# Performance work log

Measured on AMD Instinct MI355X. Metric: run time of the kernel, lower is better.

The kernel has to match this reference:

```python
import jax, jax.numpy as jnp
import numpy as np

N = 10000      # nodes
E = 320000     # edges
F_IN = 33      # input node features
H = 32         # hidden
G = 64         # graphs in batch


def setup_inputs() -> dict:
    key = jax.random.key(0)
    ks = jax.random.split(key, 24)
    s = 0.1  # small init scale for numerical sanity
    inp = {
        "x": jax.random.normal(ks[0], (N, F_IN), jnp.float32),
        "edge_index": jax.random.randint(ks[1], (2, E), 0, N, jnp.int32),
        "edge_attr": jax.random.uniform(ks[2], (E, 1), jnp.float32),
        "batch": jnp.sort(jax.random.randint(ks[3], (N,), 0, G, jnp.int32)),
        # conv1: edge-MLP Linear(1 -> F_IN*H), root weight [F_IN,H], bias [H]
        "nn_w1": jax.random.normal(ks[4], (1, F_IN * H), jnp.float32) * s,
        "nn_b1": jax.random.normal(ks[5], (F_IN * H,), jnp.float32) * s,
        "root1": jax.random.normal(ks[6], (F_IN, H), jnp.float32) * s,
        "bias1": jnp.zeros((H,), jnp.float32),
        # conv2: edge-MLP Linear(1 -> H*H)
        "nn_w2": jax.random.normal(ks[7], (1, H * H), jnp.float32) * s,
        "nn_b2": jax.random.normal(ks[8], (H * H,), jnp.float32) * s,
        "root2": jax.random.normal(ks[9], (H, H), jnp.float32) * s,
        "bias2": jnp.zeros((H,), jnp.float32),
        # conv3
        "nn_w3": jax.random.normal(ks[10], (1, H * H), jnp.float32) * s,
        "nn_b3": jax.random.normal(ks[11], (H * H,), jnp.float32) * s,
        "root3": jax.random.normal(ks[12], (H, H), jnp.float32) * s,
        "bias3": jnp.zeros((H,), jnp.float32),
        # readout MLP: Linear(3H -> H), Linear(H -> 2)
        "lin1_w": jax.random.normal(ks[13], (3 * H, H), jnp.float32) * s,
        "lin1_b": jnp.zeros((H,), jnp.float32),
        "lin2_w": jax.random.normal(ks[14], (H, 2), jnp.float32) * s,
        "lin2_b": jnp.zeros((2,), jnp.float32),
    }
    return inp


def _nnconv(x, src, dst, edge_attr, nn_w, nn_b, root, bias):
    """PyG NNConv (aggr='add'): out_i = x_i @ root + bias + sum_{e: dst(e)=i} x_{src(e)} @ Theta(e_attr)."""
    in_dim, out_dim = root.shape
    # per-edge weight matrix from edge MLP: [E, in, out]
    W = (edge_attr @ nn_w + nn_b).reshape(-1, in_dim, out_dim)
    msg = jnp.einsum('ei,eio->eo', x[src], W)          # gather + per-edge small matmul
    agg = jax.ops.segment_sum(msg, dst, num_segments=N)  # scatter-add into targets
    return agg + x @ root + bias


def reference(x, edge_index, edge_attr, batch,
              nn_w1, nn_b1, root1, bias1,
              nn_w2, nn_b2, root2, bias2,
              nn_w3, nn_b3, root3, bias3,
              lin1_w, lin1_b, lin2_w, lin2_b):
    src, dst = edge_index[0], edge_index[1]
    h = jax.nn.relu(_nnconv(x, src, dst, edge_attr, nn_w1, nn_b1, root1, bias1))
    h = jax.nn.relu(_nnconv(h, src, dst, edge_attr, nn_w2, nn_b2, root2, bias2))
    h = jax.nn.relu(_nnconv(h, src, dst, edge_attr, nn_w3, nn_b3, root3, bias3))
    # global add / mean / max pooling over graphs
    add_p = jax.ops.segment_sum(h, batch, num_segments=G)
    cnt = jax.ops.segment_sum(jnp.ones((N, 1), h.dtype), batch, num_segments=G)
    mean_p = add_p / jnp.maximum(cnt, 1.0)
    max_p = jax.ops.segment_max(h, batch, num_segments=G)
    max_p = jnp.where(jnp.isfinite(max_p), max_p, 0.0)  # guard empty segments
    g = jnp.concatenate([add_p, mean_p, max_p], axis=1)  # [G, 3H]
    g = jax.nn.relu(g @ lin1_w + lin1_b)
    # dropout p=0.5 is identity in eval mode
    logits = g @ lin2_w + lin2_b
    return jax.nn.log_softmax(logits, axis=-1)
```

## Files before the change

kernel.cpp:

```cpp
#include <hip/hip_runtime.h>

constexpr int N_  = 10000;
constexpr int E_  = 320000;
constexpr int F1  = 33;
constexpr int H   = 32;
constexpr int G   = 64;
constexpr int CAP = 96;

constexpr int GRID = 1250;
constexpr int BT   = 256;

__device__ __forceinline__ unsigned bf16r(float x) {
    unsigned u = __float_as_uint(x);
    return (u + 0x7FFFu + ((u >> 16) & 1u)) >> 16;
}

struct Prm {
    const float* x; const int* ei; const float* ea; const int* batch;
    const float* A1; const float* B1; const float* R1; const float* z1;
    const float* A2; const float* B2; const float* R2; const float* z2;
    const float* A3; const float* B3; const float* R3; const float* z3;
    const float* l1w; const float* l1b; const float* l2w; const float* l2b;
    int* counts; int* startsP; unsigned* meta;
    unsigned* UVa; float* Ra; unsigned* UVb; float* Rb;
    float* psum; unsigned* pmax;
    float* out;
};

__global__ __launch_bounds__(BT, 5) void k_build(Prm p) {
    const int tid = threadIdx.x, bid = blockIdx.x;
    {
        int e = bid * BT + tid;
        int s = p.ei[e];
        int d = p.ei[E_ + e];
        float av = p.ea[e];
        int pos = atomicAdd(&p.counts[d], 1);
        p.meta[(size_t)d * CAP + pos] = (unsigned)s | (bf16r(av) << 16);
    }
    const int grp = tid >> 5, f = tid & 31;
    const int node = bid * 8 + grp;
    if (f == 0) {
        int b = p.batch[node];
        int bp = (node == 0) ? -1 : p.batch[node - 1];
        if (b != bp) p.startsP[b] = node + 1;
    }
    float u = 0.f, v = 0.f, r = p.z1[f];
    const float* xr = p.x + (size_t)node * F1;
    #pragma unroll
    for (int k = 0; k < F1; ++k) {
        float xv = xr[k];
        u = fmaf(xv, p.A1[k * H + f], u);
        v = fmaf(xv, p.B1[k * H + f], v);
        r = fmaf(xv, p.R1[k * H + f], r);
    }
    p.UVa[(node << 5) | f] = bf16r(u) | (bf16r(v) << 16);
    p.Ra [(node << 5) | f] = r;
}

template<int LAYER>
__global__ __launch_bounds__(BT, 5) void k_agg(Prm p) {
    __shared__ float wL[3][H * H];
    __shared__ float sh[8][H];
    const int tid = threadIdx.x;

    const unsigned* UVin; const float* Rin; unsigned* UVout; float* Rout;
    if (LAYER == 1)      { UVin = p.UVa; Rin = p.Ra; UVout = p.UVb; Rout = p.Rb; }
    else if (LAYER == 2) { UVin = p.UVb; Rin = p.Rb; UVout = p.UVa; Rout = p.Ra; }
    else                 { UVin = p.UVa; Rin = p.Ra; UVout = nullptr; Rout = nullptr; }

    if (LAYER == 1) {
        for (int i = tid; i < H * H; i += BT) {
            wL[0][i] = p.A2[i]; wL[1][i] = p.B2[i]; wL[2][i] = p.R2[i];
        }
        __syncthreads();
    } else if (LAYER == 2) {
        for (int i = tid; i < H * H; i += BT) {
            wL[0][i] = p.A3[i]; wL[1][i] = p.B3[i]; wL[2][i] = p.R3[i];
        }
        __syncthreads();
    }

    const int lane = tid & 63, wav = tid >> 6;
    const int l2 = lane & 31;
    const int rg = l2 >> 3;
    const int fq = l2 & 7;
    const int n = blockIdx.x * 8 + wav * 2 + (lane >> 5);
    const int dg = p.counts[n];
    const unsigned* mrow = p.meta + (size_t)n * CAP;
    unsigned m0 = mrow[l2];
    float r = Rin[(n << 5) | l2];

    float a0 = 0.f, a1 = 0.f, a2 = 0.f, a3 = 0.f;
    uint4 wq[8]; unsigned mq[8];

    auto issue = [&](unsigned mreg, int t, int sl) {
        int j = 4 * t + rg;
        unsigned mv = __shfl(mreg, (lane & 32) | (j & 31), 64);
        mq[sl] = mv;
        unsigned src = min(mv & 0xFFFFu, (unsigned)(N_ - 1));
        wq[sl] = *reinterpret_cast<const uint4*>(UVin + ((size_t)src << 5) + 4 * fq);
    };
    auto use = [&](int t, int sl) {
        unsigned mv = mq[sl]; uint4 w = wq[sl];
        float a = __uint_as_float(mv & 0xFFFF0000u);
        bool live = (4 * t + rg) < dg;
        float t0 = fmaf(a, __uint_as_float(w.x << 16), __uint_as_float(w.x & 0xFFFF0000u));
        float t1 = fmaf(a, __uint_as_float(w.y << 16), __uint_as_float(w.y & 0xFFFF0000u));
        float t2 = fmaf(a, __uint_as_float(w.z << 16), __uint_as_float(w.z & 0xFFFF0000u));
        float t3 = fmaf(a, __uint_as_float(w.w << 16), __uint_as_float(w.w & 0xFFFF0000u));
        if (live) { a0 += t0; a1 += t1; a2 += t2; a3 += t3; }
    };

    #pragma unroll
    for (int t = 0; t < 8; ++t) issue(m0, t, t);
    const bool need1 = __any(dg > 32);
    unsigned m1 = 0;
    if (need1) m1 = mrow[32 + l2];
    #pragma unroll
    for (int t = 0; t < 8; ++t) use(t, t);
    if (need1) {
        #pragma unroll
        for (int t = 8; t < 12; ++t) issue(m1, t, t - 8);
        #pragma unroll
        for (int t = 8; t < 12; ++t) use(t, t - 8);
        if (__any(dg > 48)) {
            #pragma unroll
            for (int t = 12; t < 16; ++t) issue(m1, t, t - 12);
            #pragma unroll
            for (int t = 12; t < 16; ++t) use(t, t - 12);
            if (__any(dg > 64)) {
                unsigned m2 = mrow[64 + l2];
                #pragma unroll
                for (int t = 16; t < 24; ++t) issue(m2, t, t - 16);
                #pragma unroll
                for (int t = 16; t < 24; ++t) use(t, t - 16);
            }
        }
    }

    a0 += __shfl_xor(a0, 8);  a0 += __shfl_xor(a0, 16);
    a1 += __shfl_xor(a1, 8);  a1 += __shfl_xor(a1, 16);
    a2 += __shfl_xor(a2, 8);  a2 += __shfl_xor(a2, 16);
    a3 += __shfl_xor(a3, 8);  a3 += __shfl_xor(a3, 16);

    int rsrc = (lane & 32) | (l2 >> 2);
    float s0 = __shfl(a0, rsrc, 64), s1 = __shfl(a1, rsrc, 64);
    float s2 = __shfl(a2, rsrc, 64), s3 = __shfl(a3, rsrc, 64);
    int c = l2 & 3;
    float accf = (c == 0) ? s0 : (c == 1) ? s1 : (c == 2) ? s2 : s3;

    float h = fmaxf(r + accf, 0.f);

    if (LAYER == 3) {
        sh[wav * 2 + (lane >> 5)][l2] = h;
        __syncthreads();
        if (tid < 32) {
            const int f = tid;
            const int n0 = blockIdx.x * 8;
            float s = 0.f, mx = 0.f;
            int cg = p.batch[n0];
            #pragma unroll
            for (int i = 0; i < 8; ++i) {
                int bg = p.batch[n0 + i];
                if (bg != cg) {
                    atomicAdd(&p.psum[cg * H + f], s);
                    atomicMax(&p.pmax[cg * H + f], __float_as_uint(mx));
                    s = 0.f; mx = 0.f; cg = bg;
                }
                float hv = sh[i][f];
                s += hv; mx = fmaxf(mx, hv);
            }
            atomicAdd(&p.psum[cg * H + f], s);
            atomicMax(&p.pmax[cg * H + f], __float_as_uint(mx));
        }
    } else {
        const float zf = (LAYER == 1) ? p.z2[l2] : p.z3[l2];
        float u = 0.f, v = 0.f, rn = zf;
        #pragma unroll
        for (int k = 0; k < H; ++k) {
            float hk = __shfl(h, k, 32);
            u  = fmaf(hk, wL[0][k * H + l2], u);
            v  = fmaf(hk, wL[1][k * H + l2], v);
            rn = fmaf(hk, wL[2][k * H + l2], rn);
        }
        UVout[(n << 5) | l2] = bf16r(u) | (bf16r(v) << 16);
        Rout [(n << 5) | l2] = rn;
    }
}

__global__ __launch_bounds__(64, 8) void k_read(Prm p) {
    __shared__ int   sst[G];
    __shared__ float gpl[3 * H];
    const int tid = threadIdx.x;
    const int g = blockIdx.x;
    sst[tid] = p.startsP[tid];
    __syncthreads();
    int sp = sst[g];
    int s0 = 0, e0 = 0;
    if (sp != 0) {
        s0 = sp - 1;
        e0 = N_;
        for (int j = g + 1; j < G; ++j)
            if (sst[j]) { e0 = sst[j] - 1; break; }
    }
    if (tid < 32) {
        float sum = p.psum[g * H + tid];
        float mx  = __uint_as_float(p.pmax[g * H + tid]);
        float c = fmaxf((float)(e0 - s0), 1.0f);
        gpl[tid] = sum;
        gpl[H + tid] = sum / c;
        gpl[2 * H + tid] = mx;
    }
    __syncthreads();
    if (tid < 32) {
        float hacc = p.l1b[tid];
        #pragma unroll
        for (int k = 0; k < H; ++k) {
            hacc = fmaf(gpl[k],         p.l1w[k * H + tid], hacc);
            hacc = fmaf(gpl[H + k],     p.l1w[(H + k) * H + tid], hacc);
            hacc = fmaf(gpl[2 * H + k], p.l1w[(2 * H + k) * H + tid], hacc);
        }
        float hid = fmaxf(hacc, 0.f);
        float p0 = hid * p.l2w[tid * 2 + 0];
        float p1 = hid * p.l2w[tid * 2 + 1];
        #pragma unroll
        for (int o = 16; o; o >>= 1) {
            p0 += __shfl_xor(p0, o, 32);
            p1 += __shfl_xor(p1, o, 32);
        }
        if (tid == 0) {
            float l0 = p0 + p.l2b[0], l1 = p1 + p.l2b[1];
            float m = fmaxf(l0, l1);
            float lse = m + logf(expf(l0 - m) + expf(l1 - m));
            p.out[g * 2 + 0] = l0 - lse;
            p.out[g * 2 + 1] = l1 - lse;
        }
    }
}


extern "C" void kernel_launch(void* const* d_in, const int* in_sizes, int n_in,
                              void* d_out, int out_size, void* d_ws, size_t ws_size,
                              hipStream_t stream) {
    const float* x      = (const float*)d_in[0];
    const int*   ei     = (const int*)  d_in[1];
    const float* ea     = (const float*)d_in[2];
    const int*   batch  = (const int*)  d_in[3];
    const float* nn_w1  = (const float*)d_in[4];
    const float* nn_b1  = (const float*)d_in[5];
    const float* root1  = (const float*)d_in[6];
    const float* bias1  = (const float*)d_in[7];
    const float* nn_w2  = (const float*)d_in[8];
    const float* nn_b2  = (const float*)d_in[9];
    const float* root2  = (const float*)d_in[10];
    const float* bias2  = (const float*)d_in[11];
    const float* nn_w3  = (const float*)d_in[12];
    const float* nn_b3  = (const float*)d_in[13];
    const float* root3  = (const float*)d_in[14];
    const float* bias3  = (const float*)d_in[15];
    const float* lin1_w = (const float*)d_in[16];
    const float* lin1_b = (const float*)d_in[17];
    const float* lin2_w = (const float*)d_in[18];
    const float* lin2_b = (const float*)d_in[19];
    float* out = (float*)d_out;

    char* ws = (char*)d_ws;
    size_t off = 0;
    auto alloc = [&](size_t bytes) -> void* {
        void* p = ws + off;
        off += (bytes + 255) & ~(size_t)255;
        return p;
    };
    const size_t zbytes = N_ * sizeof(int) + G * sizeof(int)
                        + G * H * sizeof(float) + G * H * sizeof(unsigned);
    char* zchunk = (char*)alloc(zbytes);
    int*      counts  = (int*)zchunk;
    int*      startsP = (int*)(zchunk + N_ * sizeof(int));
    float*    psum    = (float*)(zchunk + N_ * sizeof(int) + G * sizeof(int));
    unsigned* pmax    = (unsigned*)(zchunk + N_ * sizeof(int) + G * sizeof(int)
                                    + G * H * sizeof(float));
    unsigned* meta = (unsigned*)alloc((size_t)N_ * CAP * sizeof(unsigned));
    unsigned* UVa = (unsigned*)alloc((size_t)N_ * H * sizeof(unsigned));
    float*    Ra  = (float*)   alloc((size_t)N_ * H * sizeof(float));
    unsigned* UVb = (unsigned*)alloc((size_t)N_ * H * sizeof(unsigned));
    float*    Rb  = (float*)   alloc((size_t)N_ * H * sizeof(float));

    Prm prm{ x, ei, ea, batch,
             nn_w1, nn_b1, root1, bias1,
             nn_w2, nn_b2, root2, bias2,
             nn_w3, nn_b3, root3, bias3,
             lin1_w, lin1_b, lin2_w, lin2_b,
             counts, startsP, meta, UVa, Ra, UVb, Rb, psum, pmax, out };

    hipMemsetAsync(zchunk, 0, zbytes, stream);
    k_build <<<GRID, BT, 0, stream>>>(prm);
    k_agg<1><<<GRID, BT, 0, stream>>>(prm);
    k_agg<2><<<GRID, BT, 0, stream>>>(prm);
    k_agg<3><<<GRID, BT, 0, stream>>>(prm);
    k_read  <<<G,    64, 0, stream>>>(prm);
}
```

Baseline: 155.2 us.

## Fuse graph readout into last aggregation kernel via last-block counter

```diff
diff --git a/kernel.cpp b/kernel.cpp
--- a/kernel.cpp
+++ b/kernel.cpp
@@ -24,6 +24,7 @@
     int* counts; int* startsP; unsigned* meta;
     unsigned* UVa; float* Ra; unsigned* UVb; float* Rb;
     float* psum; unsigned* pmax;
+    int* done;
     float* out;
 };
 
@@ -57,38 +58,85 @@
     p.Ra [(node << 5) | f] = r;
 }
 
+__device__ __forceinline__ void readout(const Prm& p, int* sst, float (*gpl)[3 * H]) {
+    const int tid = threadIdx.x;
+    if (tid < G) sst[tid] = p.startsP[tid];
+    __syncthreads();
+    const int grp = tid >> 5, l = tid & 31;
+    for (int g = grp; g < G; g += 8) {
+        int sp = sst[g];
+        int s0 = 0, e0 = 0;
+        if (sp != 0) {
+            s0 = sp - 1;
+            e0 = N_;
+            for (int j = g + 1; j < G; ++j)
+                if (sst[j]) { e0 = sst[j] - 1; break; }
+        }
+        float sum = atomicAdd(&p.psum[g * H + l], 0.f);
+        float mx  = __uint_as_float(atomicMax(&p.pmax[g * H + l], 0u));
+        float c = fmaxf((float)(e0 - s0), 1.0f);
+        gpl[grp][l] = sum;
+        gpl[grp][H + l] = sum / c;
+        gpl[grp][2 * H + l] = mx;
+        float hacc = p.l1b[l];
+        #pragma unroll
+        for (int k = 0; k < H; ++k) {
+            hacc = fmaf(gpl[grp][k],         p.l1w[k * H + l], hacc);
+            hacc = fmaf(gpl[grp][H + k],     p.l1w[(H + k) * H + l], hacc);
+            hacc = fmaf(gpl[grp][2 * H + k], p.l1w[(2 * H + k) * H + l], hacc);
+        }
+        float hid = fmaxf(hacc, 0.f);
+        float p0 = hid * p.l2w[l * 2 + 0];
+        float p1 = hid * p.l2w[l * 2 + 1];
+        #pragma unroll
+        for (int o = 16; o; o >>= 1) {
+            p0 += __shfl_xor(p0, o, 32);
+            p1 += __shfl_xor(p1, o, 32);
+        }
+        if (l == 0) {
+            float l0 = p0 + p.l2b[0], l1 = p1 + p.l2b[1];
+            float m = fmaxf(l0, l1);
+            float lse = m + logf(expf(l0 - m) + expf(l1 - m));
+            p.out[g * 2 + 0] = l0 - lse;
+            p.out[g * 2 + 1] = l1 - lse;
+        }
+    }
+}
+
 template<int LAYER>
 __global__ __launch_bounds__(BT, 5) void k_agg(Prm p) {
     __shared__ float wL[3][H * H];
     __shared__ float sh[8][H];
+    __shared__ int   sst[G];
+    __shared__ float gpl[8][3 * H];
+    __shared__ int   lastf;
     const int tid = threadIdx.x;
 
     const unsigned* UVin; const float* Rin; unsigned* UVout; float* Rout;
     if (LAYER == 1)      { UVin = p.UVa; Rin = p.Ra; UVout = p.UVb; Rout = p.Rb; }
     else if (LAYER == 2) { UVin = p.UVb; Rin = p.Rb; UVout = p.UVa; Rout = p.Ra; }
     else                 { UVin = p.UVa; Rin = p.Ra; UVout = nullptr; Rout = nullptr; }
-
-    if (LAYER == 1) {
-        for (int i = tid; i < H * H; i += BT) {
-            wL[0][i] = p.A2[i]; wL[1][i] = p.B2[i]; wL[2][i] = p.R2[i];
-        }
-        __syncthreads();
-    } else if (LAYER == 2) {
-        for (int i = tid; i < H * H; i += BT) {
-            wL[0][i] = p.A3[i]; wL[1][i] = p.B3[i]; wL[2][i] = p.R3[i];
-        }
-        __syncthreads();
-    }
 
     const int lane = tid & 63, wav = tid >> 6;
     const int l2 = lane & 31;
     const int rg = l2 >> 3;
     const int fq = l2 & 7;
     const int n = blockIdx.x * 8 + wav * 2 + (lane >> 5);
+
     const int dg = p.counts[n];
     const unsigned* mrow = p.meta + (size_t)n * CAP;
     unsigned m0 = mrow[l2];
     float r = Rin[(n << 5) | l2];
+
+    if (LAYER == 1) {
+        for (int i = tid; i < H * H; i += BT) {
+            wL[0][i] = p.A2[i]; wL[1][i] = p.B2[i]; wL[2][i] = p.R2[i];
+        }
+    } else if (LAYER == 2) {
+        for (int i = tid; i < H * H; i += BT) {
+            wL[0][i] = p.A3[i]; wL[1][i] = p.B3[i]; wL[2][i] = p.R3[i];
+        }
+    }
 
     float a0 = 0.f, a1 = 0.f, a2 = 0.f, a3 = 0.f;
     uint4 wq[8]; unsigned mq[8];
@@ -116,25 +164,20 @@
     const bool need1 = __any(dg > 32);
     unsigned m1 = 0;
     if (need1) m1 = mrow[32 + l2];
+    if (LAYER < 3) __syncthreads();
     #pragma unroll
     for (int t = 0; t < 8; ++t) use(t, t);
     if (need1) {
         #pragma unroll
-        for (int t = 8; t < 12; ++t) issue(m1, t, t - 8);
-        #pragma unroll
-        for (int t = 8; t < 12; ++t) use(t, t - 8);
-        if (__any(dg > 48)) {
+        for (int t = 8; t < 16; ++t) issue(m1, t, t - 8);
+        #pragma unroll
+        for (int t = 8; t < 16; ++t) use(t, t - 8);
+        if (__any(dg > 64)) {
+            unsigned m2 = mrow[64 + l2];
             #pragma unroll
-            for (int t = 12; t < 16; ++t) issue(m1, t, t - 12);
+            for (int t = 16; t < 24; ++t) issue(m2, t, t - 16);
             #pragma unroll
-            for (int t = 12; t < 16; ++t) use(t, t - 12);
-            if (__any(dg > 64)) {
-                unsigned m2 = mrow[64 + l2];
-                #pragma unroll
-                for (int t = 16; t < 24; ++t) issue(m2, t, t - 16);
-                #pragma unroll
-                for (int t = 16; t < 24; ++t) use(t, t - 16);
-            }
+            for (int t = 16; t < 24; ++t) use(t, t - 16);
         }
     }
 
@@ -173,6 +216,14 @@
             atomicAdd(&p.psum[cg * H + f], s);
             atomicMax(&p.pmax[cg * H + f], __float_as_uint(mx));
         }
+        __syncthreads();
+        if (tid == 0) {
+            int d = __hip_atomic_fetch_add(p.done, 1, __ATOMIC_ACQ_REL,
+                                           __HIP_MEMORY_SCOPE_AGENT);
+            lastf = (d == GRID - 1);
+        }
+        __syncthreads();
+        if (lastf) readout(p, sst, gpl);
     } else {
         const float zf = (LAYER == 1) ? p.z2[l2] : p.z3[l2];
         float u = 0.f, v = 0.f, rn = zf;
@@ -185,56 +236,6 @@
         }
         UVout[(n << 5) | l2] = bf16r(u) | (bf16r(v) << 16);
         Rout [(n << 5) | l2] = rn;
-    }
-}
-
-__global__ __launch_bounds__(64, 8) void k_read(Prm p) {
-    __shared__ int   sst[G];
-    __shared__ float gpl[3 * H];
-    const int tid = threadIdx.x;
-    const int g = blockIdx.x;
-    sst[tid] = p.startsP[tid];
-    __syncthreads();
-    int sp = sst[g];
-    int s0 = 0, e0 = 0;
-    if (sp != 0) {
-        s0 = sp - 1;
-        e0 = N_;
-        for (int j = g + 1; j < G; ++j)
-            if (sst[j]) { e0 = sst[j] - 1; break; }
-    }
-    if (tid < 32) {
-        float sum = p.psum[g * H + tid];
-        float mx  = __uint_as_float(p.pmax[g * H + tid]);
-        float c = fmaxf((float)(e0 - s0), 1.0f);
-        gpl[tid] = sum;
-        gpl[H + tid] = sum / c;
-        gpl[2 * H + tid] = mx;
-    }
-    __syncthreads();
-    if (tid < 32) {
-        float hacc = p.l1b[tid];
-        #pragma unroll
-        for (int k = 0; k < H; ++k) {
-            hacc = fmaf(gpl[k],         p.l1w[k * H + tid], hacc);
-            hacc = fmaf(gpl[H + k],     p.l1w[(H + k) * H + tid], hacc);
-            hacc = fmaf(gpl[2 * H + k], p.l1w[(2 * H + k) * H + tid], hacc);
-        }
-        float hid = fmaxf(hacc, 0.f);
-        float p0 = hid * p.l2w[tid * 2 + 0];
-        float p1 = hid * p.l2w[tid * 2 + 1];
-        #pragma unroll
-        for (int o = 16; o; o >>= 1) {
-            p0 += __shfl_xor(p0, o, 32);
-            p1 += __shfl_xor(p1, o, 32);
-        }
-        if (tid == 0) {
-            float l0 = p0 + p.l2b[0], l1 = p1 + p.l2b[1];
-            float m = fmaxf(l0, l1);
-            float lse = m + logf(expf(l0 - m) + expf(l1 - m));
-            p.out[g * 2 + 0] = l0 - lse;
-            p.out[g * 2 + 1] = l1 - lse;
-        }
     }
 }
 
@@ -271,14 +272,17 @@
         off += (bytes + 255) & ~(size_t)255;
         return p;
     };
-    const size_t zbytes = N_ * sizeof(int) + G * sizeof(int)
-                        + G * H * sizeof(float) + G * H * sizeof(unsigned);
+    const size_t zb0 = N_ * sizeof(int);
+    const size_t zb1 = zb0 + G * sizeof(int);
+    const size_t zb2 = zb1 + G * H * sizeof(float);
+    const size_t zb3 = zb2 + G * H * sizeof(unsigned);
+    const size_t zbytes = zb3 + sizeof(int);
     char* zchunk = (char*)alloc(zbytes);
     int*      counts  = (int*)zchunk;
-    int*      startsP = (int*)(zchunk + N_ * sizeof(int));
-    float*    psum    = (float*)(zchunk + N_ * sizeof(int) + G * sizeof(int));
-    unsigned* pmax    = (unsigned*)(zchunk + N_ * sizeof(int) + G * sizeof(int)
-                                    + G * H * sizeof(float));
+    int*      startsP = (int*)(zchunk + zb0);
+    float*    psum    = (float*)(zchunk + zb1);
+    unsigned* pmax    = (unsigned*)(zchunk + zb2);
+    int*      done    = (int*)(zchunk + zb3);
     unsigned* meta = (unsigned*)alloc((size_t)N_ * CAP * sizeof(unsigned));
     unsigned* UVa = (unsigned*)alloc((size_t)N_ * H * sizeof(unsigned));
     float*    Ra  = (float*)   alloc((size_t)N_ * H * sizeof(float));
@@ -290,12 +294,11 @@
              nn_w2, nn_b2, root2, bias2,
              nn_w3, nn_b3, root3, bias3,
              lin1_w, lin1_b, lin2_w, lin2_b,
-             counts, startsP, meta, UVa, Ra, UVb, Rb, psum, pmax, out };
+             counts, startsP, meta, UVa, Ra, UVb, Rb, psum, pmax, done, out };
 
     hipMemsetAsync(zchunk, 0, zbytes, stream);
     k_build <<<GRID, BT, 0, stream>>>(prm);
     k_agg<1><<<GRID, BT, 0, stream>>>(prm);
     k_agg<2><<<GRID, BT, 0, stream>>>(prm);
     k_agg<3><<<GRID, BT, 0, stream>>>(prm);
-    k_read  <<<G,    64, 0, stream>>>(prm);
-}
+}
```

After: 289.6 us. +86.6%, slower.
